# Kernel tuning notes

Hardware: AMD Instinct MI355X
Metric: run time of the kernel (lower is better)

## Reference

```python
import jax, jax.numpy as jnp
import numpy as np

B, N, D, H, DH, DFF = 2, 2048, 1024, 16, 64, 4096
EPS = 1e-5  # F.layer_norm default


def setup_inputs() -> dict:
    key = jax.random.key(0)
    ks = jax.random.split(key, 8)
    w = lambda k, shape: jax.random.normal(k, shape, dtype=jnp.float32) * 0.02
    # standard rotary frequencies over full head dim (rot_dim = DH)
    inv_freq = 1.0 / (10000.0 ** (jnp.arange(0, DH, 2, dtype=jnp.float32) / DH))
    t = jnp.arange(N, dtype=jnp.float32)
    f = t[:, None] * inv_freq[None, :]          # [N, DH/2]
    freqs = jnp.concatenate([f, f], axis=-1)    # [N, DH]
    return {
        "x": jax.random.normal(ks[0], (B, N, D), dtype=jnp.float32),
        "gamma_pre": jnp.ones((D,), jnp.float32),
        "w_qkv": w(ks[1], (3 * D, D)),
        "w_o": w(ks[2], (D, D)),
        "gamma_ff": jnp.ones((D,), jnp.float32),
        "w_up": w(ks[3], (DFF, D)),
        "b_up": jnp.zeros((DFF,), jnp.float32),
        "w_gate": w(ks[4], (DFF, D)),
        "b_gate": jnp.zeros((DFF,), jnp.float32),
        "w_out": w(ks[5], (D, DFF)),
        "b_out": jnp.zeros((D,), jnp.float32),
        "freqs": freqs,
        "mask": jnp.ones((B, N), dtype=bool),
    }


def _layernorm(x, gamma):
    mu = jnp.mean(x, axis=-1, keepdims=True)
    var = jnp.var(x, axis=-1, keepdims=True)
    return (x - mu) * jax.lax.rsqrt(var + EPS) * gamma


def _rotate_half(x):
    x1, x2 = jnp.split(x, 2, axis=-1)
    return jnp.concatenate([-x2, x1], axis=-1)


def _rope(t, freqs):
    # rot_dim == DH so nothing is left unrotated
    return t * jnp.cos(freqs) + _rotate_half(t) * jnp.sin(freqs)


def reference(x, gamma_pre, w_qkv, w_o, gamma_ff, w_up, b_up, w_gate, b_gate,
              w_out, b_out, freqs, mask):
    b, n, d = x.shape
    # ---- self-attention branch (pre-norm) ----
    h = _layernorm(x, gamma_pre)
    qkv = h @ w_qkv.T                                   # [b, n, 3d]
    q, k, v = jnp.split(qkv, 3, axis=-1)
    to_heads = lambda t: t.reshape(b, n, H, DH).transpose(0, 2, 1, 3)  # b h n d
    q, k, v = to_heads(q), to_heads(k), to_heads(v)
    q = _rope(q, freqs)
    k = _rope(k, freqs)
    scale = 1.0 / np.sqrt(DH).astype(np.float32)
    dots = jnp.einsum('bhid,bhjd->bhij', q, k) * scale  # [b, H, n, n]
    neg = -jnp.finfo(dots.dtype).max
    dots = jnp.where(mask[:, None, None, :], dots, neg)        # key padding mask
    causal = jnp.triu(jnp.ones((n, n), dtype=bool), 1)
    dots = jnp.where(causal, neg, dots)
    attn = jax.nn.softmax(dots.astype(jnp.float32), axis=-1).astype(dots.dtype)
    o = jnp.einsum('bhij,bhjd->bhid', attn, v)
    o = o.transpose(0, 2, 1, 3).reshape(b, n, d) @ w_o.T
    o = jnp.where(mask[..., None], o, 0.0)
    x = x + o
    # ---- GLU feed-forward branch (pre-norm) ----
    h2 = _layernorm(x, gamma_ff)
    up = h2 @ w_up.T + b_up
    gate = h2 @ w_gate.T + b_gate
    ff = (up * jax.nn.silu(gate)) @ w_out.T + b_out
    return x + ff
```

## Files before the change

### kernel.cpp

```cpp
#include <hip/hip_runtime.h>
#include <stdint.h>


#define B_ 2
#define N_ 2048
#define D_ 1024
#define H_ 16
#define DFF_ 4096
#define ROWS_ (B_*N_)

typedef unsigned short u16;
typedef short short4_ __attribute__((ext_vector_type(4)));
typedef short short8 __attribute__((ext_vector_type(8)));
typedef float float4_ __attribute__((ext_vector_type(4)));

#define NEGBIG (-1e30f)
#define QSCALE 0.1803368801111204f

__device__ __forceinline__ float b2f(u16 u) {
  union { unsigned u; float f; } c; c.u = ((unsigned)u) << 16; return c.f;
}
__device__ __forceinline__ u16 f2b(float f) {
  union { float f; unsigned u; } c; c.f = f;
  unsigned x = c.u;
  x += 0x7fffu + ((x >> 16) & 1u);
  return (u16)(x >> 16);
}

__device__ __forceinline__ void gl_lds16(const u16* g, u16* l) {
  __builtin_amdgcn_global_load_lds(
      (const __attribute__((address_space(1))) unsigned int*)g,
      (__attribute__((address_space(3))) unsigned int*)l, 16, 0, 0);
}

__global__ __launch_bounds__(256) void cvt_all(const float* __restrict__ s_qkv,
                                               const float* __restrict__ s_o,
                                               const float* __restrict__ s_up,
                                               const float* __restrict__ s_gate,
                                               const float* __restrict__ s_out,
                                               u16* __restrict__ d_qkv,
                                               u16* __restrict__ d_o,
                                               u16* __restrict__ d_up,
                                               u16* __restrict__ d_gate,
                                               u16* __restrict__ d_out_) {
  int c = blockIdx.x * 256 + threadIdx.x;
  const float* src; u16* dst; int off;
  if (c < 393216)       { src = s_qkv;  dst = d_qkv;  off = c; }
  else if (c < 524288)  { src = s_o;    dst = d_o;    off = c - 393216; }
  else if (c < 1048576) { src = s_up;   dst = d_up;   off = c - 524288; }
  else if (c < 1572864) { src = s_gate; dst = d_gate; off = c - 1048576; }
  else                  { src = s_out;  dst = d_out_; off = c - 1572864; }
  int i = off * 8;
  float4_ v0 = *(const float4_*)(src + i);
  float4_ v1 = *(const float4_*)(src + i + 4);
  short8 pk;
#pragma unroll
  for (int e = 0; e < 4; e++) { pk[e] = (short)f2b(v0[e]); pk[4 + e] = (short)f2b(v1[e]); }
  *(short8*)(dst + i) = pk;
}

__global__ __launch_bounds__(256) void ln_kernel(const float* __restrict__ xin,
                                                 const float* __restrict__ gamma,
                                                 u16* __restrict__ out) {
  int row = blockIdx.x, t = threadIdx.x;
  float4_ v = *(const float4_*)(xin + (size_t)row * D_ + t * 4);
  float s = 0.f, ss = 0.f;
#pragma unroll
  for (int i = 0; i < 4; i++) { s += v[i]; ss += v[i] * v[i]; }
#pragma unroll
  for (int off = 1; off < 64; off <<= 1) {
    s  += __shfl_xor(s, off, 64);
    ss += __shfl_xor(ss, off, 64);
  }
  __shared__ float red[8];
  if ((t & 63) == 0) { red[t >> 6] = s; red[4 + (t >> 6)] = ss; }
  __syncthreads();
  s  = red[0] + red[1] + red[2] + red[3];
  ss = red[4] + red[5] + red[6] + red[7];
  float mu  = s * (1.f / D_);
  float var = ss * (1.f / D_) - mu * mu;
  float rs  = rsqrtf(var + 1e-5f);
#pragma unroll
  for (int i = 0; i < 4; i++)
    out[(size_t)row * D_ + t * 4 + i] = f2b((v[i] - mu) * rs * gamma[t * 4 + i]);
}

__global__ __launch_bounds__(256) void combine_ln(const u16* p0,
                                                  const u16* __restrict__ p1,
                                                  const float* __restrict__ resid,
                                                  const float* __restrict__ gamma,
                                                  float* __restrict__ x1,
                                                  u16* h2out) {
  int row = blockIdx.x, t = threadIdx.x;
  size_t base = (size_t)row * D_ + t * 4;
  short4_ a = *(const short4_*)(p0 + base);
  short4_ b = *(const short4_*)(p1 + base);
  float4_ rv = *(const float4_*)(resid + base);
  float4_ v;
  float s = 0.f, ss = 0.f;
#pragma unroll
  for (int i = 0; i < 4; i++) {
    v[i] = b2f((u16)a[i]) + b2f((u16)b[i]) + rv[i];
    s += v[i]; ss += v[i] * v[i];
  }
  *(float4_*)(x1 + base) = v;
#pragma unroll
  for (int off = 1; off < 64; off <<= 1) {
    s  += __shfl_xor(s, off, 64);
    ss += __shfl_xor(ss, off, 64);
  }
  __shared__ float red[8];
  if ((t & 63) == 0) { red[t >> 6] = s; red[4 + (t >> 6)] = ss; }
  __syncthreads();
  s  = red[0] + red[1] + red[2] + red[3];
  ss = red[4] + red[5] + red[6] + red[7];
  float mu  = s * (1.f / D_);
  float var = ss * (1.f / D_) - mu * mu;
  float rs  = rsqrtf(var + 1e-5f);
#pragma unroll
  for (int i = 0; i < 4; i++)
    h2out[base + i] = f2b((v[i] - mu) * rs * gamma[t * 4 + i]);
}

template <int MODE>
__device__ __forceinline__ void gemm_epilogue(float4_ (&acc)[4][4], void* Cout,
                                              const float* bias, const void* extra,
                                              int mbase, int nbase, int N,
                                              int wr, int wc, int quad, int l16) {
#pragma unroll
  for (int i = 0; i < 4; i++) {
#pragma unroll
    for (int r = 0; r < 4; r++) {
      int row = mbase + wr * 64 + i * 16 + quad * 4 + r;
#pragma unroll
      for (int j = 0; j < 4; j++) {
        int col = nbase + wc * 64 + j * 16 + l16;
        size_t idx = (size_t)row * N + col;
        float v = acc[i][j][r];
        if (MODE == 0) {
          ((u16*)Cout)[idx] = f2b(v);
        } else if (MODE == 1) {
          ((u16*)Cout)[idx] = f2b(v + bias[col]);
        } else if (MODE == 2) {
          ((float*)Cout)[idx] = v + ((const float*)extra)[idx];
        } else if (MODE == 3) {
          float gate = v + bias[col];
          float sig = 1.f / (1.f + expf(-gate));
          float upv = b2f(((const u16*)extra)[idx]);
          ((u16*)Cout)[idx] = f2b(upv * gate * sig);
        } else {
          ((float*)Cout)[idx] = v + bias[col] + ((const float*)extra)[idx];
        }
      }
    }
  }
}

__global__ __launch_bounds__(256) void gemm_bb_split(const u16* __restrict__ A,
                                                     const u16* __restrict__ W,
                                                     u16* __restrict__ p0,
                                                     u16* __restrict__ p1,
                                                     int M, int N, int K) {
  __shared__ __align__(16) u16 ring[4][8192];
  int t_ = threadIdx.x, wave = t_ >> 6, lane = t_ & 63;
  int wr = wave >> 1, wc = wave & 1;
  int quad = lane >> 4, l16 = lane & 15;
  int mbase = blockIdx.y * 128, nbase = blockIdx.x * 128;
  int z = blockIdx.z;
  int Kh = K >> 1, kbase = z * Kh;
  const int NT = Kh >> 5;
  int colb = ((lane & 3) ^ ((lane >> 3) & 3)) << 3;
  int qs8  = (quad ^ ((l16 >> 1) & 3)) * 8;

  float4_ z4 = {0.f, 0.f, 0.f, 0.f};
  float4_ acc[4][4];
#pragma unroll
  for (int i = 0; i < 4; i++)
#pragma unroll
    for (int j = 0; j < 4; j++) acc[i][j] = z4;

  auto STAGE = [&](int kk) {
    u16* sl = &ring[kk & 3][0];
    int kc = kbase + kk * 32 + colb;
#pragma unroll
    for (int it = 0; it < 2; it++) {
      int c = it * 256 + wave * 64 + lane;
      int row = c >> 2;
      gl_lds16(A + (size_t)(mbase + row) * K + kc, sl + (it * 256 + wave * 64) * 8);
      gl_lds16(W + (size_t)(nbase + row) * K + kc, sl + 4096 + (it * 256 + wave * 64) * 8);
    }
  };
  auto READF = [&](short8 (&fa)[4], short8 (&fb)[4], int kk) {
    const u16* sl = &ring[kk & 3][0];
#pragma unroll
    for (int i = 0; i < 4; i++)
      fa[i] = *(const short8*)(sl + (wr * 64 + i * 16 + l16) * 32 + qs8);
#pragma unroll
    for (int j = 0; j < 4; j++)
      fb[j] = *(const short8*)(sl + 4096 + (wc * 64 + j * 16 + l16) * 32 + qs8);
  };
  auto MM = [&](short8 (&fa)[4], short8 (&fb)[4]) {
    __builtin_amdgcn_s_setprio(1);
#pragma unroll
    for (int i = 0; i < 4; i++)
#pragma unroll
      for (int j = 0; j < 4; j++)
        acc[i][j] = __builtin_amdgcn_mfma_f32_16x16x32_bf16(fa[i], fb[j], acc[i][j], 0, 0, 0);
    __builtin_amdgcn_s_setprio(0);
  };

  STAGE(0); STAGE(1); STAGE(2);
  asm volatile("s_waitcnt vmcnt(8)" ::: "memory");
  __builtin_amdgcn_s_barrier();
  asm volatile("" ::: "memory");
  short8 aX[4], bX[4], aY[4], bY[4];
  READF(aX, bX, 0);

  auto ITER = [&](int t, short8 (&ca)[4], short8 (&cb)[4],
                  short8 (&na)[4], short8 (&nb)[4]) {
    if (t + 3 < NT) STAGE(t + 3);
    if (t + 1 < NT) {
      if (t + 3 < NT)      asm volatile("s_waitcnt vmcnt(8)" ::: "memory");
      else if (t + 2 < NT) asm volatile("s_waitcnt vmcnt(4)" ::: "memory");
      else                 asm volatile("s_waitcnt vmcnt(0)" ::: "memory");
      __builtin_amdgcn_s_barrier();
      asm volatile("" ::: "memory");
      READF(na, nb, t + 1);
    }
    MM(ca, cb);
    if (t + 1 < NT) { __builtin_amdgcn_s_barrier(); asm volatile("" ::: "memory"); }
  };
  for (int t = 0; t < NT; t += 2) {
    ITER(t, aX, bX, aY, bY);
    ITER(t + 1, aY, bY, aX, bX);
  }

  u16* P = z ? p1 : p0;
#pragma unroll
  for (int i = 0; i < 4; i++)
#pragma unroll
    for (int r = 0; r < 4; r++) {
      int row = mbase + wr * 64 + i * 16 + quad * 4 + r;
#pragma unroll
      for (int j = 0; j < 4; j++) {
        int col = nbase + wc * 64 + j * 16 + l16;
        P[(size_t)row * N + col] = f2b(acc[i][j][r]);
      }
    }
}

__global__ __launch_bounds__(512) void gemm_glu8(const u16* __restrict__ A,
                                                 const u16* __restrict__ Wu,
                                                 const u16* __restrict__ Wg,
                                                 const float* __restrict__ bu,
                                                 const float* __restrict__ bg,
                                                 u16* __restrict__ G) {
  __shared__ __align__(16) u16 ring[4][16384];
  const int NT = 32;
  int t_ = threadIdx.x, wave = t_ >> 6, lane = t_ & 63;
  int wr = wave >> 2, wc = wave & 3;
  int quad = lane >> 4, l16 = lane & 15;
  int mbase = blockIdx.y * 256, nbase = blockIdx.x * 128;
  int colb = ((lane & 3) ^ ((lane >> 3) & 3)) << 3;
  int qs8  = (quad ^ ((l16 >> 1) & 3)) * 8;

  float4_ z4 = {0.f, 0.f, 0.f, 0.f};
  float4_ acc[8][4];
#pragma unroll
  for (int i = 0; i < 8; i++)
#pragma unroll
    for (int j = 0; j < 4; j++) acc[i][j] = z4;

  auto STAGE = [&](int kk) {
    u16* sl = &ring[kk & 3][0];
    int rw = wave * 16 + (lane >> 2);
    int kc = kk * 32 + colb;
#pragma unroll
    for (int it = 0; it < 2; it++)
      gl_lds16(A + (size_t)(mbase + it * 128 + rw) * 1024 + kc,
               sl + it * 4096 + wave * 512);
    size_t go = (size_t)(nbase + rw) * 1024 + kc;
    gl_lds16(Wu + go, sl + 8192 + wave * 512);
    gl_lds16(Wg + go, sl + 12288 + wave * 512);
  };
  auto READF = [&](short8 (&fa)[8], short8 (&fb)[4], int kk) {
    const u16* as = &ring[kk & 3][0];
    const u16* bs = as + 8192;
#pragma unroll
    for (int i = 0; i < 8; i++)
      fa[i] = *(const short8*)(as + (wr * 128 + i * 16 + l16) * 32 + qs8);
#pragma unroll
    for (int j = 0; j < 4; j++)
      fb[j] = *(const short8*)(bs + (wc * 64 + j * 16 + l16) * 32 + qs8);
  };
  auto MM = [&](short8 (&fa)[8], short8 (&fb)[4]) {
    __builtin_amdgcn_s_setprio(1);
#pragma unroll
    for (int i = 0; i < 8; i++)
#pragma unroll
      for (int j = 0; j < 4; j++)
        acc[i][j] = __builtin_amdgcn_mfma_f32_16x16x32_bf16(fa[i], fb[j], acc[i][j], 0, 0, 0);
    __builtin_amdgcn_s_setprio(0);
  };

  STAGE(0); STAGE(1); STAGE(2);
  asm volatile("s_waitcnt vmcnt(8)" ::: "memory");
  __builtin_amdgcn_s_barrier();
  asm volatile("" ::: "memory");
  short8 aX[8], bX[4], aY[8], bY[4];
  READF(aX, bX, 0);

  auto ITER = [&](int t, short8 (&ca)[8], short8 (&cb)[4],
                  short8 (&na)[8], short8 (&nb)[4]) {
    if (t + 3 < NT) STAGE(t + 3);
    if (t + 1 < NT) {
      if (t + 3 < NT)      asm volatile("s_waitcnt vmcnt(8)" ::: "memory");
      else if (t + 2 < NT) asm volatile("s_waitcnt vmcnt(4)" ::: "memory");
      else                 asm volatile("s_waitcnt vmcnt(0)" ::: "memory");
      __builtin_amdgcn_s_barrier();
      asm volatile("" ::: "memory");
      READF(na, nb, t + 1);
    }
    MM(ca, cb);
    if (t + 1 < NT) { __builtin_amdgcn_s_barrier(); asm volatile("" ::: "memory"); }
  };
  for (int t = 0; t < NT; t += 2) {
    ITER(t, aX, bX, aY, bY);
    ITER(t + 1, aY, bY, aX, bX);
  }

  __syncthreads();
  u16* ex = &ring[0][0];
  if (wc >= 2) {
    int cc = (wc - 2) * 64;
#pragma unroll
    for (int i = 0; i < 8; i++)
#pragma unroll
      for (int r = 0; r < 4; r++) {
        int row = wr * 128 + i * 16 + quad * 4 + r;
#pragma unroll
        for (int j = 0; j < 4; j++) {
          int col = cc + j * 16 + l16;
          float gv = acc[i][j][r] + bg[nbase + col];
          float sig = 1.f / (1.f + expf(-gv));
          ex[row * 128 + col] = f2b(gv * sig);
        }
      }
  }
  __syncthreads();
  if (wc < 2) {
    int cc = wc * 64;
#pragma unroll
    for (int i = 0; i < 8; i++)
#pragma unroll
      for (int r = 0; r < 4; r++) {
        int row = wr * 128 + i * 16 + quad * 4 + r;
#pragma unroll
        for (int j = 0; j < 4; j++) {
          int col = cc + j * 16 + l16;
          float uv = acc[i][j][r] + bu[nbase + col];
          G[(size_t)(mbase + row) * DFF_ + nbase + col] =
              f2b(uv * b2f(ex[row * 128 + col]));
        }
      }
  }
}

__global__ __launch_bounds__(256) void split_combine(const u16* __restrict__ p0,
                                                     const u16* __restrict__ p1,
                                                     const float* __restrict__ bias,
                                                     const float* __restrict__ resid,
                                                     float* __restrict__ out, int N) {
  int idx = (blockIdx.x * 256 + threadIdx.x) * 8;
  int col = idx & (N - 1);
  short8 a = *(const short8*)(p0 + idx);
  short8 b = *(const short8*)(p1 + idx);
  float4_ r0 = *(const float4_*)(resid + idx);
  float4_ r1 = *(const float4_*)(resid + idx + 4);
  float4_ o0, o1;
#pragma unroll
  for (int e = 0; e < 4; e++) {
    float bb0 = bias ? bias[col + e] : 0.f;
    float bb1 = bias ? bias[col + 4 + e] : 0.f;
    o0[e] = b2f((u16)a[e]) + b2f((u16)b[e]) + bb0 + r0[e];
    o1[e] = b2f((u16)a[4 + e]) + b2f((u16)b[4 + e]) + bb1 + r1[e];
  }
  *(float4_*)(out + idx) = o0;
  *(float4_*)(out + idx + 4) = o1;
}

template <int MODE>
__global__ __launch_bounds__(256) void gemm_nt(const u16* __restrict__ A,
                                               const float* __restrict__ W,
                                               void* Cout,
                                               const float* __restrict__ bias,
                                               const void* extra,
                                               int M, int N, int K) {
  __shared__ __align__(16) u16 sA[128 * 32];
  __shared__ __align__(16) u16 sW[128 * 32];
  int t = threadIdx.x;
  int mbase = blockIdx.y * 128, nbase = blockIdx.x * 128;
  int wave = t >> 6, lane = t & 63;
  int wr = wave >> 1, wc = wave & 1;
  int quad = lane >> 4, l16 = lane & 15;

  float4_ z4 = {0.f, 0.f, 0.f, 0.f};
  float4_ acc[4][4];
#pragma unroll
  for (int i = 0; i < 4; i++)
#pragma unroll
    for (int j = 0; j < 4; j++) acc[i][j] = z4;

  for (int k0 = 0; k0 < K; k0 += 32) {
    __syncthreads();
#pragma unroll
    for (int it = 0; it < 2; it++) {
      int c = t + 256 * it;
      int row = c >> 2, col = (c & 3) << 3;
      ((short8*)sA)[c] = *(const short8*)(A + (size_t)(mbase + row) * K + k0 + col);
      const float* wp = W + (size_t)(nbase + row) * K + k0 + col;
      float4_ w0 = *(const float4_*)wp;
      float4_ w1 = *(const float4_*)(wp + 4);
      short8 pk;
#pragma unroll
      for (int e = 0; e < 4; e++) { pk[e] = (short)f2b(w0[e]); pk[4 + e] = (short)f2b(w1[e]); }
      ((short8*)sW)[c] = pk;
    }
    __syncthreads();
    short8 af[4], bf[4];
#pragma unroll
    for (int i = 0; i < 4; i++)
      af[i] = *(const short8*)(sA + (wr * 64 + i * 16 + l16) * 32 + quad * 8);
#pragma unroll
    for (int j = 0; j < 4; j++)
      bf[j] = *(const short8*)(sW + (wc * 64 + j * 16 + l16) * 32 + quad * 8);
#pragma unroll
    for (int i = 0; i < 4; i++)
#pragma unroll
      for (int j = 0; j < 4; j++)
        acc[i][j] = __builtin_amdgcn_mfma_f32_16x16x32_bf16(af[i], bf[j], acc[i][j], 0, 0, 0);
  }
  gemm_epilogue<MODE>(acc, Cout, bias, extra, mbase, nbase, N, wr, wc, quad, l16);
}

template <int SPLIT>
__global__ __launch_bounds__(256) void rope_kernel(const u16* __restrict__ q0,
                                                   const u16* __restrict__ q1,
                                                   const float* __restrict__ freqs,
                                                   u16* __restrict__ qr,
                                                   u16* __restrict__ kr,
                                                   u16* __restrict__ vt) {
  int idx = blockIdx.x * 256 + threadIdx.x;
  int d2 = idx & 31;
  int h  = (idx >> 5) & 15;
  int n  = (idx >> 9) & 2047;
  int b  = idx >> 20;
  float f = freqs[n * 64 + d2];
  float c = cosf(f), s = sinf(f);
  size_t base = (size_t)(b * N_ + n) * 3072;
  int hd = h * 64 + d2;
#define LD(o) (SPLIT ? (b2f(q0[base + (o)]) + b2f(q1[base + (o)])) : b2f(q0[base + (o)]))
  float v_q1 = LD(hd),        v_q2 = LD(hd + 32);
  float v_k1 = LD(1024 + hd), v_k2 = LD(1024 + hd + 32);
  float v_v1 = LD(2048 + hd), v_v2 = LD(2048 + hd + 32);
#undef LD
  size_t ro = ((size_t)(b * H_ + h) * N_ + n) * 64 + d2;
  qr[ro]      = f2b((v_q1 * c - v_q2 * s) * QSCALE);
  qr[ro + 32] = f2b((v_q2 * c + v_q1 * s) * QSCALE);
  kr[ro]      = f2b(v_k1 * c - v_k2 * s);
  kr[ro + 32] = f2b(v_k2 * c + v_k1 * s);
  size_t vo = ((size_t)(b * H_ + h) * 64 + d2) * N_ + n;
  vt[vo]           = f2b(v_v1);
  vt[vo + 32 * N_] = f2b(v_v2);
}

#define LP 72
#define NSPLIT 4
__global__ __launch_bounds__(256) void attn_kernel(const u16* __restrict__ qr,
                                                   const u16* __restrict__ kr,
                                                   const u16* __restrict__ vt,
                                                   u16* __restrict__ opart,
                                                   float* __restrict__ mlp) {
  __shared__ __align__(16) u16 sK[64 * LP];
  __shared__ __align__(16) u16 sV[64 * LP];
  __shared__ __align__(16) u16 sP[4][16 * LP];
  int qp = blockIdx.x, bh = blockIdx.y, sp = blockIdx.z;
  int t = threadIdx.x, wave = t >> 6, lane = t & 63;
  int quad = lane >> 4, l16 = lane & 15;
  const u16* qptr = qr + (size_t)bh * N_ * 64;
  const u16* kp = kr + (size_t)bh * N_ * 64;
  const u16* vp = vt + (size_t)bh * 64 * N_;
  float4_ z4 = {0.f, 0.f, 0.f, 0.f};

  for (int qsel = 0; qsel < 2; qsel++) {
    int qt = qsel ? (N_ / 64 - 1 - qp) : qp;
    int qbase = qt * 64;
    int ntiles = qt + 1;
    int ktlo = (ntiles * sp) / NSPLIT, kthi = (ntiles * (sp + 1)) / NSPLIT;

    short8 aq[2];
    int qrow = qbase + wave * 16 + l16;
#pragma unroll
    for (int kk = 0; kk < 2; kk++)
      aq[kk] = *(const short8*)(qptr + (size_t)qrow * 64 + kk * 32 + quad * 8);

    float4_ o[4] = {z4, z4, z4, z4};
    float m_r[4] = {NEGBIG, NEGBIG, NEGBIG, NEGBIG};
    float l_r[4] = {0.f, 0.f, 0.f, 0.f};

    for (int kt = ktlo; kt < kthi; kt++) {
      __syncthreads();
      {
        const u16* src = kp + (size_t)kt * 64 * 64;
#pragma unroll
        for (int it = 0; it < 2; it++) {
          int c = t + 256 * it;
          int row = c >> 3, seg = c & 7;
          *(short8*)(sK + row * LP + seg * 8) = *(const short8*)(src + c * 8);
          *(short8*)(sV + row * LP + seg * 8) =
              *(const short8*)(vp + (size_t)row * N_ + kt * 64 + seg * 8);
        }
      }
      __syncthreads();

      float4_ sf[4];
#pragma unroll
      for (int j = 0; j < 4; j++) {
        short8 bk0 = *(const short8*)(sK + (j * 16 + l16) * LP + quad * 8);
        short8 bk1 = *(const short8*)(sK + (j * 16 + l16) * LP + 32 + quad * 8);
        float4_ acc = z4;
        acc = __builtin_amdgcn_mfma_f32_16x16x32_bf16(aq[0], bk0, acc, 0, 0, 0);
        acc = __builtin_amdgcn_mfma_f32_16x16x32_bf16(aq[1], bk1, acc, 0, 0, 0);
        sf[j] = acc;
      }
      if (kt == qt) {
#pragma unroll
        for (int j = 0; j < 4; j++)
#pragma unroll
          for (int r = 0; r < 4; r++) {
            int ig = qbase + wave * 16 + quad * 4 + r;
            int jg = kt * 64 + j * 16 + l16;
            if (jg > ig) sf[j][r] = NEGBIG;
          }
      }

#pragma unroll
      for (int r = 0; r < 4; r++) {
        float mt = fmaxf(fmaxf(sf[0][r], sf[1][r]), fmaxf(sf[2][r], sf[3][r]));
#pragma unroll
        for (int off = 1; off < 16; off <<= 1) mt = fmaxf(mt, __shfl_xor(mt, off, 64));
        float mn = fmaxf(m_r[r], mt);
        float alpha = exp2f(m_r[r] - mn);
        float rowsum = 0.f;
#pragma unroll
        for (int j = 0; j < 4; j++) {
          float p = exp2f(sf[j][r] - mn);
          sf[j][r] = p;
          rowsum += p;
        }
#pragma unroll
        for (int off = 1; off < 16; off <<= 1) rowsum += __shfl_xor(rowsum, off, 64);
        l_r[r] = l_r[r] * alpha + rowsum;
        m_r[r] = mn;
#pragma unroll
        for (int jo = 0; jo < 4; jo++) o[jo][r] *= alpha;
      }

      u16* sPw = sP[wave];
#pragma unroll
      for (int j = 0; j < 4; j++)
#pragma unroll
        for (int r = 0; r < 4; r++)
          sPw[(quad * 4 + r) * LP + j * 16 + l16] = f2b(sf[j][r]);
      short8 ap[2];
#pragma unroll
      for (int kk = 0; kk < 2; kk++)
        ap[kk] = *(const short8*)(sPw + l16 * LP + kk * 32 + quad * 8);
#pragma unroll
      for (int jo = 0; jo < 4; jo++)
#pragma unroll
        for (int kk = 0; kk < 2; kk++) {
          short8 bv = *(const short8*)(sV + (jo * 16 + l16) * LP + kk * 32 + quad * 8);
          o[jo] = __builtin_amdgcn_mfma_f32_16x16x32_bf16(ap[kk], bv, o[jo], 0, 0, 0);
        }
    }

#pragma unroll
    for (int r = 0; r < 4; r++) {
      int n = qbase + wave * 16 + quad * 4 + r;
      size_t row = (size_t)bh * N_ + n;
      if (l16 == 0) {
        mlp[2 * (sp * (size_t)65536 + row)]     = m_r[r];
        mlp[2 * (sp * (size_t)65536 + row) + 1] = l_r[r];
      }
#pragma unroll
      for (int jo = 0; jo < 4; jo++)
        opart[sp * (size_t)4194304 + row * 64 + jo * 16 + l16] = f2b(o[jo][r]);
    }
  }
}

__global__ __launch_bounds__(256) void attn_combine(const u16* __restrict__ opart,
                                                    const float* __restrict__ mlp,
                                                    u16* __restrict__ obuf) {
  int idx = blockIdx.x * 256 + threadIdx.x;
  int row = idx >> 3, seg = idx & 7;
  float mm[NSPLIT], ll[NSPLIT];
  float mmax = NEGBIG;
#pragma unroll
  for (int s = 0; s < NSPLIT; s++) {
    mm[s] = mlp[2 * (s * (size_t)65536 + row)];
    ll[s] = mlp[2 * (s * (size_t)65536 + row) + 1];
    mmax = fmaxf(mmax, mm[s]);
  }
  float w[NSPLIT], lsum = 0.f;
#pragma unroll
  for (int s = 0; s < NSPLIT; s++) { w[s] = exp2f(mm[s] - mmax); lsum += ll[s] * w[s]; }
  float inv = 1.f / lsum;
  float acc[8] = {0, 0, 0, 0, 0, 0, 0, 0};
#pragma unroll
  for (int s = 0; s < NSPLIT; s++) {
    short8 a = *(const short8*)(opart + s * (size_t)4194304 + (size_t)row * 64 + seg * 8);
#pragma unroll
    for (int e = 0; e < 8; e++) acc[e] += b2f((u16)a[e]) * w[s];
  }
  short8 r;
#pragma unroll
  for (int e = 0; e < 8; e++) r[e] = (short)f2b(acc[e] * inv);
  int bh = row >> 11, n = row & 2047;
  int bb = bh >> 4, h = bh & 15;
  *(short8*)(obuf + ((size_t)(bb * N_ + n) * D_) + h * 64 + seg * 8) = r;
}

extern "C" void kernel_launch(void* const* d_in, const int* in_sizes, int n_in,
                              void* d_out, int out_size, void* d_ws, size_t ws_size,
                              hipStream_t stream) {
  const float* x         = (const float*)d_in[0];
  const float* gamma_pre = (const float*)d_in[1];
  const float* w_qkv     = (const float*)d_in[2];
  const float* w_o       = (const float*)d_in[3];
  const float* gamma_ff  = (const float*)d_in[4];
  const float* w_up      = (const float*)d_in[5];
  const float* b_up      = (const float*)d_in[6];
  const float* w_gate    = (const float*)d_in[7];
  const float* b_gate    = (const float*)d_in[8];
  const float* w_out     = (const float*)d_in[9];
  const float* b_out     = (const float*)d_in[10];
  const float* freqs     = (const float*)d_in[11];

  char* ws = (char*)d_ws;
  const size_t MB = 1024 * 1024;
  float* out = (float*)d_out;
  bool wide = ws_size >= 96 * MB;

  if (wide) {
    u16*  h     = (u16*)(ws);
    u16*  qp0   = (u16*)(ws + 8 * MB);
    u16*  qp1   = (u16*)(ws + 32 * MB);
    u16*  qr    = (u16*)(ws + 56 * MB);
    u16*  kr    = (u16*)d_out;
    u16*  vtb   = (u16*)d_out + 4194304;
    u16*  opart = (u16*)(ws);
    float* mlb  = (float*)(ws + 32 * MB);
    u16*  ob    = (u16*)(ws + 34 * MB);
    u16*  sp0   = (u16*)(ws);
    u16*  sp1o  = (u16*)(ws + 8 * MB);
    float* x1   = (float*)(ws + 16 * MB);
    u16*  h2    = (u16*)(ws);
    u16*  g     = (u16*)(ws + 32 * MB);
    u16*  sp0f  = (u16*)(ws);
    u16*  sp1f  = (u16*)(ws + 8 * MB);
    u16* wb_qkv  = (u16*)(ws + 64 * MB);
    u16* wb_o    = (u16*)(ws + 70 * MB);
    u16* wb_up   = (u16*)(ws + 72 * MB);
    u16* wb_gate = (u16*)(ws + 80 * MB);
    u16* wb_out  = (u16*)(ws + 88 * MB);

    cvt_all<<<8192, 256, 0, stream>>>(w_qkv, w_o, w_up, w_gate, w_out,
                                      wb_qkv, wb_o, wb_up, wb_gate, wb_out);
    ln_kernel<<<ROWS_, 256, 0, stream>>>(x, gamma_pre, h);
    gemm_bb_split<<<dim3(3072 / 128, ROWS_ / 128, 2), 256, 0, stream>>>(
        h, wb_qkv, qp0, qp1, ROWS_, 3072, 1024);
    rope_kernel<1><<<(B_ * N_ * H_ * 32) / 256, 256, 0, stream>>>(
        qp0, qp1, freqs, qr, kr, vtb);
    attn_kernel<<<dim3(N_ / 128, B_ * H_, NSPLIT), 256, 0, stream>>>(
        qr, kr, vtb, opart, mlb);
    attn_combine<<<(B_ * H_ * N_ * 8) / 256, 256, 0, stream>>>(opart, mlb, ob);
    gemm_bb_split<<<dim3(1024 / 128, ROWS_ / 128, 2), 256, 0, stream>>>(
        ob, wb_o, sp0, sp1o, ROWS_, 1024, 1024);
    combine_ln<<<ROWS_, 256, 0, stream>>>(sp0, sp1o, x, gamma_ff, x1, h2);
    gemm_glu8<<<dim3(DFF_ / 128, ROWS_ / 256), 512, 0, stream>>>(
        h2, wb_up, wb_gate, b_up, b_gate, g);
    gemm_bb_split<<<dim3(1024 / 128, ROWS_ / 128, 2), 256, 0, stream>>>(
        g, wb_out, sp0f, sp1f, ROWS_, 1024, 4096);
    split_combine<<<(ROWS_ * 1024) / 2048, 256, 0, stream>>>(
        sp0f, sp1f, b_out, x1, out, 1024);
  } else {
    u16*  h     = (u16*)(ws);
    u16*  qkv   = (u16*)(ws + 8 * MB);
    u16*  qr    = (u16*)(ws + 32 * MB);
    u16*  kr    = (u16*)(ws + 40 * MB);
    u16*  vtb   = (u16*)(ws + 48 * MB);
    u16*  ob    = (u16*)(ws + 56 * MB);
    float* x1   = (float*)(ws + 8 * MB);
    u16*  h2    = (u16*)(ws + 24 * MB);
    u16*  g     = (u16*)(ws + 32 * MB);

    ln_kernel<<<ROWS_, 256, 0, stream>>>(x, gamma_pre, h);
    gemm_nt<0><<<dim3(3072 / 128, ROWS_ / 128), 256, 0, stream>>>(
        h, w_qkv, qkv, nullptr, nullptr, ROWS_, 3072, 1024);
    rope_kernel<0><<<(B_ * N_ * H_ * 32) / 256, 256, 0, stream>>>(
        qkv, qkv, freqs, qr, kr, vtb);
    attn_kernel<<<dim3(N_ / 128, B_ * H_, NSPLIT), 256, 0, stream>>>(
        qr, kr, vtb, (u16*)(ws), (float*)(ws + 32 * MB));
    attn_combine<<<(B_ * H_ * N_ * 8) / 256, 256, 0, stream>>>(
        (u16*)(ws), (float*)(ws + 32 * MB), ob);
    gemm_nt<2><<<dim3(1024 / 128, ROWS_ / 128), 256, 0, stream>>>(
        ob, w_o, x1, nullptr, x, ROWS_, 1024, 1024);
    ln_kernel<<<ROWS_, 256, 0, stream>>>(x1, gamma_ff, h2);
    gemm_nt<1><<<dim3(4096 / 128, ROWS_ / 128), 256, 0, stream>>>(
        h2, w_up, g, b_up, nullptr, ROWS_, 4096, 1024);
    gemm_nt<3><<<dim3(4096 / 128, ROWS_ / 128), 256, 0, stream>>>(
        h2, w_gate, g, b_gate, g, ROWS_, 4096, 1024);
    gemm_nt<4><<<dim3(1024 / 128, ROWS_ / 128), 256, 0, stream>>>(
        g, w_out, (void*)out, b_out, x1, ROWS_, 1024, 4096);
  }
}
```

Baseline: 471.0 us.

## Restructure GEMM main loops into single-buffered register fragments with split staging

The generic GEMM and the GLU GEMM drop double-buffered register fragments (prefetching the next tile's LDS reads during the current MFMAs). Each iteration now reads its own fragments from LDS, issues global prefetch, barriers, waits on LDS, then runs MFMAs. The GLU kernel splits its K-step into two half-phases, issuing the A-tile and the W-tile global loads separately so memory traffic is interleaved with two MFMA bursts. This lowers register pressure, which may allow higher occupancy or fewer spills. The cost is more barriers and exposed LDS latency before each MFMA burst, since fragment loads no longer overlap compute.

```diff
diff --git a/kernel.cpp b/kernel.cpp
--- a/kernel.cpp
+++ b/kernel.cpp
@@ -190,49 +190,37 @@
       gl_lds16(W + (size_t)(nbase + row) * K + kc, sl + 4096 + (it * 256 + wave * 64) * 8);
     }
   };
-  auto READF = [&](short8 (&fa)[4], short8 (&fb)[4], int kk) {
-    const u16* sl = &ring[kk & 3][0];
-#pragma unroll
-    for (int i = 0; i < 4; i++)
-      fa[i] = *(const short8*)(sl + (wr * 64 + i * 16 + l16) * 32 + qs8);
-#pragma unroll
-    for (int j = 0; j < 4; j++)
-      fb[j] = *(const short8*)(sl + 4096 + (wc * 64 + j * 16 + l16) * 32 + qs8);
-  };
-  auto MM = [&](short8 (&fa)[4], short8 (&fb)[4]) {
-    __builtin_amdgcn_s_setprio(1);
-#pragma unroll
-    for (int i = 0; i < 4; i++)
-#pragma unroll
-      for (int j = 0; j < 4; j++)
-        acc[i][j] = __builtin_amdgcn_mfma_f32_16x16x32_bf16(fa[i], fb[j], acc[i][j], 0, 0, 0);
-    __builtin_amdgcn_s_setprio(0);
-  };
 
   STAGE(0); STAGE(1); STAGE(2);
   asm volatile("s_waitcnt vmcnt(8)" ::: "memory");
   __builtin_amdgcn_s_barrier();
-  asm volatile("" ::: "memory");
-  short8 aX[4], bX[4], aY[4], bY[4];
-  READF(aX, bX, 0);
-
-  auto ITER = [&](int t, short8 (&ca)[4], short8 (&cb)[4],
-                  short8 (&na)[4], short8 (&nb)[4]) {
+
+  for (int t = 0; t < NT; t++) {
+    const u16* sl = &ring[t & 3][0];
+    short8 af[4], bf[4];
+#pragma unroll
+    for (int i = 0; i < 4; i++)
+      af[i] = *(const short8*)(sl + (wr * 64 + i * 16 + l16) * 32 + qs8);
+#pragma unroll
+    for (int j = 0; j < 4; j++)
+      bf[j] = *(const short8*)(sl + 4096 + (wc * 64 + j * 16 + l16) * 32 + qs8);
     if (t + 3 < NT) STAGE(t + 3);
     if (t + 1 < NT) {
-      if (t + 3 < NT)      asm volatile("s_waitcnt vmcnt(8)" ::: "memory");
-      else if (t + 2 < NT) asm volatile("s_waitcnt vmcnt(4)" ::: "memory");
-      else                 asm volatile("s_waitcnt vmcnt(0)" ::: "memory");
-      __builtin_amdgcn_s_barrier();
-      asm volatile("" ::: "memory");
-      READF(na, nb, t + 1);
+      if (t <= NT - 4)       asm volatile("s_waitcnt vmcnt(8)" ::: "memory");
+      else if (t == NT - 3)  asm volatile("s_waitcnt vmcnt(4)" ::: "memory");
+      else                   asm volatile("s_waitcnt vmcnt(0)" ::: "memory");
     }
-    MM(ca, cb);
-    if (t + 1 < NT) { __builtin_amdgcn_s_barrier(); asm volatile("" ::: "memory"); }
-  };
-  for (int t = 0; t < NT; t += 2) {
-    ITER(t, aX, bX, aY, bY);
-    ITER(t + 1, aY, bY, aX, bX);
+    __builtin_amdgcn_s_barrier();
+    asm volatile("s_waitcnt lgkmcnt(0)" ::: "memory");
+    __builtin_amdgcn_sched_barrier(0);
+    __builtin_amdgcn_s_setprio(1);
+#pragma unroll
+    for (int i = 0; i < 4; i++)
+#pragma unroll
+      for (int j = 0; j < 4; j++)
+        acc[i][j] = __builtin_amdgcn_mfma_f32_16x16x32_bf16(af[i], bf[j], acc[i][j], 0, 0, 0);
+    __builtin_amdgcn_s_setprio(0);
+    __builtin_amdgcn_s_barrier();
   }
 
   u16* P = z ? p1 : p0;
@@ -271,7 +259,7 @@
 #pragma unroll
     for (int j = 0; j < 4; j++) acc[i][j] = z4;
 
-  auto STAGE = [&](int kk) {
+  auto STAGE_A = [&](int kk) {
     u16* sl = &ring[kk & 3][0];
     int rw = wave * 16 + (lane >> 2);
     int kc = kk * 32 + colb;
@@ -279,54 +267,66 @@
     for (int it = 0; it < 2; it++)
       gl_lds16(A + (size_t)(mbase + it * 128 + rw) * 1024 + kc,
                sl + it * 4096 + wave * 512);
-    size_t go = (size_t)(nbase + rw) * 1024 + kc;
+  };
+  auto STAGE_B = [&](int kk) {
+    u16* sl = &ring[kk & 3][0];
+    int rw = wave * 16 + (lane >> 2);
+    size_t go = (size_t)(nbase + rw) * 1024 + kk * 32 + colb;
     gl_lds16(Wu + go, sl + 8192 + wave * 512);
     gl_lds16(Wg + go, sl + 12288 + wave * 512);
   };
-  auto READF = [&](short8 (&fa)[8], short8 (&fb)[4], int kk) {
-    const u16* as = &ring[kk & 3][0];
-    const u16* bs = as + 8192;
-#pragma unroll
-    for (int i = 0; i < 8; i++)
-      fa[i] = *(const short8*)(as + (wr * 128 + i * 16 + l16) * 32 + qs8);
-#pragma unroll
-    for (int j = 0; j < 4; j++)
-      fb[j] = *(const short8*)(bs + (wc * 64 + j * 16 + l16) * 32 + qs8);
-  };
-  auto MM = [&](short8 (&fa)[8], short8 (&fb)[4]) {
-    __builtin_amdgcn_s_setprio(1);
-#pragma unroll
-    for (int i = 0; i < 8; i++)
-#pragma unroll
-      for (int j = 0; j < 4; j++)
-        acc[i][j] = __builtin_amdgcn_mfma_f32_16x16x32_bf16(fa[i], fb[j], acc[i][j], 0, 0, 0);
-    __builtin_amdgcn_s_setprio(0);
-  };
-
-  STAGE(0); STAGE(1); STAGE(2);
+
+#pragma unroll
+  for (int kk = 0; kk < 3; kk++) { STAGE_A(kk); STAGE_B(kk); }
   asm volatile("s_waitcnt vmcnt(8)" ::: "memory");
   __builtin_amdgcn_s_barrier();
-  asm volatile("" ::: "memory");
-  short8 aX[8], bX[4], aY[8], bY[4];
-  READF(aX, bX, 0);
-
-  auto ITER = [&](int t, short8 (&ca)[8], short8 (&cb)[4],
-                  short8 (&na)[8], short8 (&nb)[4]) {
-    if (t + 3 < NT) STAGE(t + 3);
+
+  for (int t = 0; t < NT; t++) {
+    const u16* as = &ring[t & 3][0];
+    const u16* bs = as + 8192;
+    bool pf = (t + 3 < NT);
+
+    short8 af[4], bf[4];
+#pragma unroll
+    for (int i = 0; i < 4; i++)
+      af[i] = *(const short8*)(as + (wr * 128 + i * 16 + l16) * 32 + qs8);
+#pragma unroll
+    for (int j = 0; j < 4; j++)
+      bf[j] = *(const short8*)(bs + (wc * 64 + j * 16 + l16) * 32 + qs8);
+    if (pf) STAGE_A(t + 3);
+    __builtin_amdgcn_s_barrier();
+    asm volatile("s_waitcnt lgkmcnt(0)" ::: "memory");
+    __builtin_amdgcn_sched_barrier(0);
+    __builtin_amdgcn_s_setprio(1);
+#pragma unroll
+    for (int i = 0; i < 4; i++)
+#pragma unroll
+      for (int j = 0; j < 4; j++)
+        acc[i][j] = __builtin_amdgcn_mfma_f32_16x16x32_bf16(af[i], bf[j], acc[i][j], 0, 0, 0);
+    __builtin_amdgcn_s_setprio(0);
+    __builtin_amdgcn_s_barrier();
+
+    short8 ag[4];
+#pragma unroll
+    for (int i = 0; i < 4; i++)
+      ag[i] = *(const short8*)(as + (wr * 128 + (4 + i) * 16 + l16) * 32 + qs8);
+    if (pf) STAGE_B(t + 3);
     if (t + 1 < NT) {
-      if (t + 3 < NT)      asm volatile("s_waitcnt vmcnt(8)" ::: "memory");
-      else if (t + 2 < NT) asm volatile("s_waitcnt vmcnt(4)" ::: "memory");
-      else                 asm volatile("s_waitcnt vmcnt(0)" ::: "memory");
-      __builtin_amdgcn_s_barrier();
-      asm volatile("" ::: "memory");
-      READF(na, nb, t + 1);
+      if (t <= NT - 4)       asm volatile("s_waitcnt vmcnt(8)" ::: "memory");
+      else if (t == NT - 3)  asm volatile("s_waitcnt vmcnt(4)" ::: "memory");
+      else                   asm volatile("s_waitcnt vmcnt(0)" ::: "memory");
     }
-    MM(ca, cb);
-    if (t + 1 < NT) { __builtin_amdgcn_s_barrier(); asm volatile("" ::: "memory"); }
-  };
-  for (int t = 0; t < NT; t += 2) {
-    ITER(t, aX, bX, aY, bY);
-    ITER(t + 1, aY, bY, aX, bX);
+    __builtin_amdgcn_s_barrier();
+    asm volatile("s_waitcnt lgkmcnt(0)" ::: "memory");
+    __builtin_amdgcn_sched_barrier(0);
+    __builtin_amdgcn_s_setprio(1);
+#pragma unroll
+    for (int i = 0; i < 4; i++)
+#pragma unroll
+      for (int j = 0; j < 4; j++)
+        acc[4 + i][j] = __builtin_amdgcn_mfma_f32_16x16x32_bf16(ag[i], bf[j], acc[4 + i][j], 0, 0, 0);
+    __builtin_amdgcn_s_setprio(0);
+    __builtin_amdgcn_s_barrier();
   }
 
   __syncthreads();
```

After: 458.1 us. 1.03x faster.
